# Optimization experiments

Measured on AMD Instinct MI355X. Metric: run time of the kernel, lower is better.

The kernel has to match this reference:

```python
import jax, jax.numpy as jnp
import numpy as np

T, B, D = 799, 8, 512
H, HD = 8, 64
M = 6                       # memory length (one per segment from prev layer)
SUMMARY = M + 1             # summary length = mem_length + 1
U = 768                     # utterance length = max(lengths)
R = T - U - SUMMARY         # right-context blocks length = 24
KL = M + R + U              # key length = 798
MAX_REL = 64
SCALE = HD ** -0.5
STD_SCALE = 0.5
NEG_INF = float('-inf')


def setup_inputs() -> dict:
    key = jax.random.key(0)
    ks = jax.random.split(key, 10)
    x = jax.random.normal(ks[0], (T, B, D), dtype=jnp.float32)
    mems = jax.random.normal(ks[1], (M, B, D), dtype=jnp.float32)
    lengths = jax.random.randint(ks[2], (B,), 400, U + 1).at[0].set(U).astype(jnp.int32)
    attention_mask = jax.random.bernoulli(ks[3], 0.1, (T, KL))  # True = masked
    rpe = jax.random.randint(ks[4], (T, KL), 0, 2 * MAX_REL + 1)
    wq = jax.random.normal(ks[5], (D, D), dtype=jnp.float32) * 0.02
    bq = jnp.zeros((D,), jnp.float32)
    wkv = jax.random.normal(ks[6], (2 * D, D), dtype=jnp.float32) * 0.02
    bkv = jnp.zeros((2 * D,), jnp.float32)
    wo = jax.random.normal(ks[7], (D, D), dtype=jnp.float32) * 0.02
    bo = jnp.zeros((D,), jnp.float32)
    rpe_k_emb = jax.random.normal(ks[8], (2 * MAX_REL + 1, HD), dtype=jnp.float32) * 0.05
    rpe_v_emb = jax.random.normal(ks[9], (2 * MAX_REL + 1, HD), dtype=jnp.float32) * 0.05
    return dict(x=x, lengths=lengths, mems=mems, attention_mask=attention_mask,
                rpe=rpe, utterance_length=U, wq=wq, bq=bq, wkv=wkv, bkv=bkv,
                wo=wo, bo=bo, rpe_k_emb=rpe_k_emb, rpe_v_emb=rpe_v_emb)


def attention_suppression(w, scale):
    # w: [B*H, T, KL] raw (masked) scores; weak-attention suppression per fairseq
    prob = jax.nn.softmax(w, axis=-1)
    nz = prob != 0.0
    nz_sum = jnp.sum(nz.astype(w.dtype), axis=-1, keepdims=True)
    key_sum = jnp.sum(prob, axis=-1, keepdims=True)
    key_mean = key_sum / (nz_sum + 1e-8)
    dis = jnp.where(nz, (prob - key_mean) * (prob - key_mean), 0.0)
    key_var = jnp.sum(dis, axis=-1, keepdims=True) / (nz_sum - 1.0 + 1e-8)
    key_thread = key_mean - scale * jnp.sqrt(key_var)
    return jnp.where(prob < key_thread, NEG_INF, w)


def reference(x, lengths, mems, attention_mask, rpe, utterance_length,
              wq, bq, wkv, bkv, wo, bo, rpe_k_emb, rpe_v_emb):
    summary_length = mems.shape[0] + 1
    rcb_len = T - utterance_length - summary_length  # right-context blocks
    rc_block = x[:rcb_len]
    utt_block = x[rcb_len:T - summary_length]
    # key-side padding mask: klengths = lengths + mem + right-context (lc=0)
    klengths = lengths + mems.shape[0] + rcb_len
    padding_mask = jnp.arange(KL)[None, :] >= klengths[:, None]  # [B, KL]
    mem_rc = jnp.concatenate([mems, rc_block, utt_block], axis=0)  # [KL, B, D]
    # projections (torch Linear: y = x @ W.T + b)
    q = jnp.einsum('tbd,ed->tbe', x, wq) + bq            # [T, B, D]
    kv = jnp.einsum('kbd,ed->kbe', mem_rc, wkv) + bkv    # [KL, B, 2D]
    k, v = jnp.split(kv, 2, axis=2)
    # heads: [T, B*H, HD] -> [B*H, T, HD]
    qh = jnp.transpose(q.reshape(T, B * H, HD), (1, 0, 2)) * SCALE
    kh = jnp.transpose(k.reshape(KL, B * H, HD), (1, 0, 2))
    vh = jnp.transpose(v.reshape(KL, B * H, HD), (1, 0, 2))
    aw = jnp.einsum('nth,nkh->ntk', qh, kh)              # [B*H, T, KL]
    # relative position bias on keys
    r_k = rpe_k_emb[rpe]                                 # [T, KL, HD]
    aw = aw + jnp.einsum('nth,tkh->ntk', qh, r_k)
    # attention mask (broadcast over B*H)
    aw = jnp.where(attention_mask[None, :, :], NEG_INF, aw)
    # key padding mask
    aw = aw.reshape(B, H, T, KL)
    aw = jnp.where(padding_mask[:, None, None, :], NEG_INF, aw)
    aw = aw.reshape(B * H, T, KL)
    # weak attention suppression (std_scale)
    aw = attention_suppression(aw, STD_SCALE)
    probs = jax.nn.softmax(aw, axis=-1)                  # dropout p=0
    attn = jnp.einsum('ntk,nkh->nth', probs, vh)         # [B*H, T, HD]
    r_v = rpe_v_emb[rpe]                                 # [T, KL, HD]
    attn_rpe = jnp.einsum('ntk,tkh->nth', probs, r_v)
    attn = 2.0 * attn + attn_rpe                          # rpe_old_option: attn += attn + rpe
    attn = jnp.transpose(attn, (1, 0, 2)).reshape(T, B, D)
    rc_output_memory = jnp.einsum('tbd,ed->tbe', attn, wo) + bo
    # use_mem, not mini_batches: next_m = out[-summary:-1], tanh squash
    next_m = jnp.tanh(rc_output_memory[T - summary_length:T - 1])
    rc_output = rc_output_memory[:T - summary_length]
    # concatenate the two live outputs into one array [T-1, B, D]
    return jnp.concatenate([rc_output, next_m], axis=0)
```

## Files before the change

kernel.cpp:

```cpp
#include <hip/hip_runtime.h>
#include <hip/hip_bf16.h>
#include <math.h>

#define TT   799
#define BB   8
#define DD   512
#define HH   8
#define HDD  64
#define MMEM 6
#define RRCB 24
#define KLL  798
#define TQ   798
#define NROWS (TQ * BB)
#define NHEADS 64
#define NEG_INF (-INFINITY)

#define TB   16
#define CH   64
#define NCH  13
#define VTS  832
#define NTCH 50
#define MINCH 7

static_assert(NROWS == 6384, "");

typedef __attribute__((ext_vector_type(8))) short short8;
typedef __attribute__((ext_vector_type(4))) float f32x4;

__device__ __forceinline__ unsigned short f2bf(float x) {
    union { float f; unsigned u; } c; c.f = x;
    unsigned r = c.u + 0x7FFFu + ((c.u >> 16) & 1u);
    return (unsigned short)(r >> 16);
}
__device__ __forceinline__ float bf2f(unsigned short b) {
    union { unsigned u; float f; } c; c.u = ((unsigned)b) << 16; return c.f;
}

__global__ void detect_mask_kernel(const unsigned int* __restrict__ a,
                                   int* __restrict__ mode)
{
    __shared__ int c0s, cHs;
    if (threadIdx.x == 0) { c0s = 0; cHs = 0; }
    __syncthreads();
    int c0 = 0, cH = 0;
    const int ND = 4096;
    for (int i = threadIdx.x; i < ND; i += blockDim.x) {
        unsigned int w = a[i];
        if (w & 0x000000FFu) c0++;
        if (w & 0xFFFFFF00u) cH++;
    }
    atomicAdd(&c0s, c0); atomicAdd(&cHs, cH);
    __syncthreads();
    if (threadIdx.x == 0)
        *mode = (cHs == 0) ? 0 : ((c0s == 0) ? 1 : 2);
}

#define RK_BLOCKS 36
#define PK2_BLOCKS (NTCH * 13)
__global__ __launch_bounds__(256)
void prep_kernel(const void* __restrict__ amask,
                 const int* __restrict__ rpe,
                 const int* __restrict__ mode_p,
                 unsigned int* __restrict__ pk2,
                 const float* __restrict__ rpe_k,
                 unsigned short* __restrict__ rk_hi,
                 unsigned short* __restrict__ rk_lo,
                 const float* __restrict__ x,
                 const float* __restrict__ mems,
                 const float* __restrict__ wq,
                 const float* __restrict__ wkv,
                 const float* __restrict__ wo,
                 unsigned short* __restrict__ xs_hi, unsigned short* __restrict__ xs_lo,
                 unsigned short* __restrict__ ms_hi, unsigned short* __restrict__ ms_lo,
                 unsigned short* __restrict__ w_hi,  unsigned short* __restrict__ w_lo)
{
    const int bid = blockIdx.x;
    const int tid = threadIdx.x;
    if (bid < PK2_BLOCKS) {
        const int mode = *mode_p;
        const int chunk = bid / 13;
        const int kg = bid - chunk * 13;
        const int k64 = tid >> 2;
        const int word = tid & 3;
        const int key = kg * 64 + k64;
        unsigned out = 0;
        #pragma unroll
        for (int r = 0; r < 4; ++r) {
            const int row = word * 4 + r;
            const int t = chunk * 16 + row;
            unsigned byte = 255u;
            if (key < KLL && t < TT) {
                size_t idx = (size_t)t * KLL + key;
                bool masked;
                if (mode == 0)      masked = (((const int*)amask)[idx] != 0);
                else if (mode == 1) masked = (((const float*)amask)[idx] != 0.f);
                else                masked = (((const unsigned char*)amask)[idx] != 0);
                byte = masked ? 255u : (unsigned)rpe[idx];
            }
            out |= byte << (8 * r);
        }
        pk2[((size_t)chunk * 832 + key) * 4 + word] = out;
    } else if (bid < PK2_BLOCKS + RK_BLOCKS) {
        int i = (bid - PK2_BLOCKS) * 256 + tid;
        if (i >= 144 * 64) return;
        int c = i >> 6;
        float v = (c < 129) ? rpe_k[i] : 0.f;
        unsigned short hi = f2bf(v);
        rk_hi[i] = hi;
        rk_lo[i] = f2bf(v - bf2f(hi));
    } else {
        const size_t NX = (size_t)NROWS * DD;
        const size_t NM = 48 * DD;
        const size_t NW = 2048 * DD;
        size_t i = ((size_t)(bid - PK2_BLOCKS - RK_BLOCKS) * 256 + tid) * 4;
        float4 v4; unsigned short *dh, *dl; size_t o;
        if (i < NX) { o = i; v4 = *(const float4*)(x + o); dh = xs_hi; dl = xs_lo; }
        else if (i < NX + NM) { o = i - NX; v4 = *(const float4*)(mems + o); dh = ms_hi; dl = ms_lo; }
        else if (i < NX + NM + NW) {
            o = i - NX - NM;
            size_t r = o >> 9;
            if (r < 512)       v4 = *(const float4*)(wq + o);
            else if (r < 1536) v4 = *(const float4*)(wkv + (o - (size_t)512 * DD));
            else               v4 = *(const float4*)(wo + (o - (size_t)1536 * DD));
            dh = w_hi; dl = w_lo;
        } else return;
        ushort4 h, lo;
        h.x = f2bf(v4.x); lo.x = f2bf(v4.x - bf2f(h.x));
        h.y = f2bf(v4.y); lo.y = f2bf(v4.y - bf2f(h.y));
        h.z = f2bf(v4.z); lo.z = f2bf(v4.z - bf2f(h.z));
        h.w = f2bf(v4.w); lo.w = f2bf(v4.w - bf2f(h.w));
        *(ushort4*)(dh + o) = h;
        *(ushort4*)(dl + o) = lo;
    }
}

__global__ __launch_bounds__(256)
void transpose_v_kernel(const unsigned short* __restrict__ vr_hi,
                        const unsigned short* __restrict__ vr_lo,
                        unsigned short* __restrict__ vt_hi,
                        unsigned short* __restrict__ vt_lo)
{
    const int head = blockIdx.y;
    const int kb = blockIdx.x * 64;
    __shared__ unsigned short th[64][66];
    __shared__ unsigned short tl[64][66];
    const int tid = threadIdx.x;
    for (int i = tid; i < 64 * 64; i += 256) {
        int ky = i >> 6, hd = i & 63;
        int key = kb + ky;
        unsigned short hv = 0, lv = 0;
        if (key < KLL) {
            size_t o = ((size_t)head * KLL + key) * HDD + hd;
            hv = vr_hi[o]; lv = vr_lo[o];
        }
        th[ky][hd] = hv; tl[ky][hd] = lv;
    }
    __syncthreads();
    for (int i = tid; i < 64 * 64; i += 256) {
        int hd = i >> 6, ky = i & 63;
        size_t o = ((size_t)head * HDD + hd) * VTS + kb + ky;
        vt_hi[o] = th[ky][hd];
        vt_lo[o] = tl[ky][hd];
    }
}

__global__ __launch_bounds__(256, 4)
void proj_qkv(const unsigned short* __restrict__ xs_hi,
              const unsigned short* __restrict__ xs_lo,
              const unsigned short* __restrict__ ms_hi,
              const unsigned short* __restrict__ ms_lo,
              const unsigned short* __restrict__ w_hi,
              const unsigned short* __restrict__ w_lo,
              const float* __restrict__ bq,
              const float* __restrict__ bkv,
              unsigned short* __restrict__ q_hi, unsigned short* __restrict__ q_lo,
              unsigned short* __restrict__ k_hi, unsigned short* __restrict__ k_lo,
              unsigned short* __restrict__ vr_hi, unsigned short* __restrict__ vr_lo)
{
    const int tid = threadIdx.x;
    const int wv = tid >> 6;
    const int quad = (tid >> 4) & 3;
    const int colk = tid & 15;
    const int m0 = blockIdx.x * 128;
    const int ny = blockIdx.y;
    const bool qpath = ny < 8;
    const int n0l = (qpath ? ny : ny - 8) * 64;
    const int wr0 = qpath ? n0l : 512 + n0l;

    __shared__ unsigned short wls_h[2][64][40];
    __shared__ unsigned short wls_l[2][64][40];

    const int sn = tid >> 2;
    const int sk = (tid & 3) * 8;
    const unsigned short* wsrc_h = w_hi + (size_t)(wr0 + sn) * DD + sk;
    const unsigned short* wsrc_l = w_lo + (size_t)(wr0 + sn) * DD + sk;

    const int amA = min(m0 + wv * 16 + colk, NROWS - 1);
    const int amB = min(m0 + 64 + wv * 16 + colk, NROWS - 1);
    const unsigned short *arhA, *arlA, *arhB, *arlB;
    if (qpath) {
        arhA = xs_hi + (size_t)amA * DD; arlA = xs_lo + (size_t)amA * DD;
        arhB = xs_hi + (size_t)amB * DD; arlB = xs_lo + (size_t)amB * DD;
    } else {
        if (amA < 48) { arhA = ms_hi + (size_t)amA * DD; arlA = ms_lo + (size_t)amA * DD; }
        else          { arhA = xs_hi + (size_t)(amA - 48) * DD; arlA = xs_lo + (size_t)(amA - 48) * DD; }
        if (amB < 48) { arhB = ms_hi + (size_t)amB * DD; arlB = ms_lo + (size_t)amB * DD; }
        else          { arhB = xs_hi + (size_t)(amB - 48) * DD; arlB = xs_lo + (size_t)(amB - 48) * DD; }
    }

    f32x4 acc[2][4] = {{{0,0,0,0},{0,0,0,0},{0,0,0,0},{0,0,0,0}},
                       {{0,0,0,0},{0,0,0,0},{0,0,0,0},{0,0,0,0}}};

    {
        short8 sh = *(const short8*)(wsrc_h);
        short8 sl = *(const short8*)(wsrc_l);
        *(short8*)&wls_h[0][sn][sk] = sh;
        *(short8*)&wls_l[0][sn][sk] = sl;
    }
    __syncthreads();

    #pragma unroll 2
    for (int ks = 0; ks < 16; ++ks) {
        const int buf = ks & 1;
        const int k0 = ks * 32;
        short8 nh, nl;
        if (ks + 1 < 16) {
            nh = *(const short8*)(wsrc_h + k0 + 32);
            nl = *(const short8*)(wsrc_l + k0 + 32);
        }
        short8 ahA = *(const short8*)(arhA + k0 + quad * 8);
        short8 alA = *(const short8*)(arlA + k0 + quad * 8);
        short8 ahB = *(const short8*)(arhB + k0 + quad * 8);
        short8 alB = *(const short8*)(arlB + k0 + quad * 8);
        #pragma unroll
        for (int nt = 0; nt < 4; ++nt) {
            short8 bh = *(const short8*)&wls_h[buf][nt * 16 + colk][quad * 8];
            short8 bl = *(const short8*)&wls_l[buf][nt * 16 + colk][quad * 8];
            acc[0][nt] = __builtin_amdgcn_mfma_f32_16x16x32_bf16(ahA, bh, acc[0][nt], 0, 0, 0);
            acc[0][nt] = __builtin_amdgcn_mfma_f32_16x16x32_bf16(ahA, bl, acc[0][nt], 0, 0, 0);
            acc[0][nt] = __builtin_amdgcn_mfma_f32_16x16x32_bf16(alA, bh, acc[0][nt], 0, 0, 0);
            acc[1][nt] = __builtin_amdgcn_mfma_f32_16x16x32_bf16(ahB, bh, acc[1][nt], 0, 0, 0);
            acc[1][nt] = __builtin_amdgcn_mfma_f32_16x16x32_bf16(ahB, bl, acc[1][nt], 0, 0, 0);
            acc[1][nt] = __builtin_amdgcn_mfma_f32_16x16x32_bf16(alB, bh, acc[1][nt], 0, 0, 0);
        }
        if (ks + 1 < 16) {
            *(short8*)&wls_h[buf ^ 1][sn][sk] = nh;
            *(short8*)&wls_l[buf ^ 1][sn][sk] = nl;
        }
        __syncthreads();
    }

    #pragma unroll
    for (int half = 0; half < 2; ++half) {
        #pragma unroll
        for (int nt = 0; nt < 4; ++nt) {
            const int nn = n0l + nt * 16 + colk;
            const float bv = qpath ? bq[nn] : bkv[nn];
            #pragma unroll
            for (int reg = 0; reg < 4; ++reg) {
                const int m = m0 + half * 64 + wv * 16 + quad * 4 + reg;
                if (m >= NROWS) continue;
                float v = acc[half][nt][reg] + bv;
                int row = m >> 3, bb = m & 7;
                if (qpath) {
                    v *= 0.125f;
                    int hh = nn >> 6, hd = nn & 63;
                    size_t o = ((size_t)(bb * HH + hh) * TQ + row) * HDD + hd;
                    unsigned short hi = f2bf(v);
                    q_hi[o] = hi; q_lo[o] = f2bf(v - bf2f(hi));
                } else if (nn < DD) {
                    int hh = nn >> 6, hd = nn & 63;
                    size_t o = ((size_t)(bb * HH + hh) * KLL + row) * HDD + hd;
                    unsigned short hi = f2bf(v);
                    k_hi[o] = hi; k_lo[o] = f2bf(v - bf2f(hi));
                } else {
                    int n2 = nn - DD;
                    int hh = n2 >> 6, hd = n2 & 63;
                    size_t o = ((size_t)(bb * HH + hh) * KLL + row) * HDD + hd;
                    unsigned short hi = f2bf(v);
                    vr_hi[o] = hi; vr_lo[o] = f2bf(v - bf2f(hi));
                }
            }
        }
    }
}

__global__ __launch_bounds__(256, 4)
void proj_out(const unsigned short* __restrict__ a_hi,
              const unsigned short* __restrict__ a_lo,
              const unsigned short* __restrict__ w_hi,
              const unsigned short* __restrict__ w_lo,
              const float* __restrict__ bias,
              float* __restrict__ out_f)
{
    const int tid = threadIdx.x;
    const int wv = tid >> 6;
    const int quad = (tid >> 4) & 3;
    const int colk = tid & 15;
    const int m0 = blockIdx.x * 128;
    const int n0 = blockIdx.y * 64;

    __shared__ unsigned short wls_h[2][64][40];
    __shared__ unsigned short wls_l[2][64][40];

    const int sn = tid >> 2;
    const int sk = (tid & 3) * 8;
    const unsigned short* wsrc_h = w_hi + (size_t)(n0 + sn) * DD + sk;
    const unsigned short* wsrc_l = w_lo + (size_t)(n0 + sn) * DD + sk;

    const int amA = min(m0 + wv * 16 + colk, NROWS - 1);
    const int amB = min(m0 + 64 + wv * 16 + colk, NROWS - 1);
    const unsigned short* arhA = a_hi + (size_t)amA * DD;
    const unsigned short* arlA = a_lo + (size_t)amA * DD;
    const unsigned short* arhB = a_hi + (size_t)amB * DD;
    const unsigned short* arlB = a_lo + (size_t)amB * DD;

    f32x4 acc[2][4] = {{{0,0,0,0},{0,0,0,0},{0,0,0,0},{0,0,0,0}},
                       {{0,0,0,0},{0,0,0,0},{0,0,0,0},{0,0,0,0}}};

    {
        short8 sh = *(const short8*)(wsrc_h);
        short8 sl = *(const short8*)(wsrc_l);
        *(short8*)&wls_h[0][sn][sk] = sh;
        *(short8*)&wls_l[0][sn][sk] = sl;
    }
    __syncthreads();

    #pragma unroll 2
    for (int ks = 0; ks < 16; ++ks) {
        const int buf = ks & 1;
        const int k0 = ks * 32;
        short8 nh, nl;
        if (ks + 1 < 16) {
            nh = *(const short8*)(wsrc_h + k0 + 32);
            nl = *(const short8*)(wsrc_l + k0 + 32);
        }
        short8 ahA = *(const short8*)(arhA + k0 + quad * 8);
        short8 alA = *(const short8*)(arlA + k0 + quad * 8);
        short8 ahB = *(const short8*)(arhB + k0 + quad * 8);
        short8 alB = *(const short8*)(arlB + k0 + quad * 8);
        #pragma unroll
        for (int nt = 0; nt < 4; ++nt) {
            short8 bh = *(const short8*)&wls_h[buf][nt * 16 + colk][quad * 8];
            short8 bl = *(const short8*)&wls_l[buf][nt * 16 + colk][quad * 8];
            acc[0][nt] = __builtin_amdgcn_mfma_f32_16x16x32_bf16(ahA, bh, acc[0][nt], 0, 0, 0);
            acc[0][nt] = __builtin_amdgcn_mfma_f32_16x16x32_bf16(ahA, bl, acc[0][nt], 0, 0, 0);
            acc[0][nt] = __builtin_amdgcn_mfma_f32_16x16x32_bf16(alA, bh, acc[0][nt], 0, 0, 0);
            acc[1][nt] = __builtin_amdgcn_mfma_f32_16x16x32_bf16(ahB, bh, acc[1][nt], 0, 0, 0);
            acc[1][nt] = __builtin_amdgcn_mfma_f32_16x16x32_bf16(ahB, bl, acc[1][nt], 0, 0, 0);
            acc[1][nt] = __builtin_amdgcn_mfma_f32_16x16x32_bf16(alB, bh, acc[1][nt], 0, 0, 0);
        }
        if (ks + 1 < 16) {
            *(short8*)&wls_h[buf ^ 1][sn][sk] = nh;
            *(short8*)&wls_l[buf ^ 1][sn][sk] = nl;
        }
        __syncthreads();
    }

    #pragma unroll
    for (int half = 0; half < 2; ++half) {
        #pragma unroll
        for (int nt = 0; nt < 4; ++nt) {
            const int nn = n0 + nt * 16 + colk;
            const float bv = bias[nn];
            #pragma unroll
            for (int reg = 0; reg < 4; ++reg) {
                const int m = m0 + half * 64 + wv * 16 + quad * 4 + reg;
                if (m >= NROWS) continue;
                float v = acc[half][nt][reg] + bv;
                int row = m >> 3;
                if (row >= TQ - MMEM) v = tanhf(v);
                out_f[(size_t)m * DD + nn] = v;
            }
        }
    }
}

__global__ __launch_bounds__(256, 3)
void attn_kernel(const unsigned short* __restrict__ qh_g,
                 const unsigned short* __restrict__ ql_g,
                 const unsigned short* __restrict__ kh_g,
                 const unsigned short* __restrict__ kl_g,
                 const unsigned short* __restrict__ vt_hi,
                 const unsigned short* __restrict__ vt_lo,
                 const int* __restrict__ lengths,
                 const unsigned int* __restrict__ pk2,
                 const unsigned short* __restrict__ rk_hi,
                 const unsigned short* __restrict__ rk_lo,
                 const float* __restrict__ rpe_v,
                 unsigned short* __restrict__ ao_hi,
                 unsigned short* __restrict__ ao_lo)
{
    const int id = blockIdx.x;
    const int xcd = id & 7;
    const int grp = id >> 3;
    const int t_chunk = grp % NTCH;
    const int n = (grp / NTCH) * 8 + xcd;
    const int t0 = t_chunk * TB;
    const int rows = min(TB, TQ - t0);
    const int b = n >> 3;
    const int h = n & 7;
    const int tid = threadIdx.x;
    const int wv = tid >> 6;
    const int quad = (tid >> 4) & 3;
    const int colk = tid & 15;
    const int myk = wv * 16 + colk;

    __shared__ float qrk_l[TB][132];
    __shared__ unsigned short p_hi[2][TB][72];
    __shared__ unsigned short p_lo[2][TB][72];
    __shared__ float4 stats_l[4][TB];

    const int klen = lengths[b] + MMEM + RRCB;
    const int nch_live = (klen + CH - 1) / CH;
    const unsigned* pkg = pk2 + (size_t)t_chunk * 832 * 4;

#define LIVE(c) ((c) < MINCH || (c) < nch_live)

    const int qrow = t0 + min(colk, rows - 1);
    const size_t qo = ((size_t)n * TQ + qrow) * HDD;
    short8 ah0 = *(const short8*)(qh_g + qo + quad * 8);
    short8 ah1 = *(const short8*)(qh_g + qo + 32 + quad * 8);
    short8 al0 = *(const short8*)(ql_g + qo + quad * 8);
    short8 al1 = *(const short8*)(ql_g + qo + 32 + quad * 8);

    for (int t = wv; t < 9; t += 4) {
        const size_t rb = (size_t)(t * 16 + colk) * 64;
        short8 bh0 = *(const short8*)(rk_hi + rb + quad * 8);
        short8 bh1 = *(const short8*)(rk_hi + rb + 32 + quad * 8);
        short8 bl0 = *(const short8*)(rk_lo + rb + quad * 8);
        short8 bl1 = *(const short8*)(rk_lo + rb + 32 + quad * 8);
        f32x4 c4 = {0.f, 0.f, 0.f, 0.f};
        c4 = __builtin_amdgcn_mfma_f32_16x16x32_bf16(ah0, bh0, c4, 0, 0, 0);
        c4 = __builtin_amdgcn_mfma_f32_16x16x32_bf16(ah1, bh1, c4, 0, 0, 0);
        c4 = __builtin_amdgcn_mfma_f32_16x16x32_bf16(ah0, bl0, c4, 0, 0, 0);
        c4 = __builtin_amdgcn_mfma_f32_16x16x32_bf16(ah1, bl1, c4, 0, 0, 0);
        c4 = __builtin_amdgcn_mfma_f32_16x16x32_bf16(al0, bh0, c4, 0, 0, 0);
        c4 = __builtin_amdgcn_mfma_f32_16x16x32_bf16(al1, bh1, c4, 0, 0, 0);
        int c = t * 16 + colk;
        if (c <= 128) {
            #pragma unroll
            for (int reg = 0; reg < 4; ++reg) qrk_l[quad * 4 + reg][c] = c4[reg];
        }
    }
    __syncthreads();

    float s_reg[NCH][4];
    float mx[4] = {-1e30f, -1e30f, -1e30f, -1e30f};

    #pragma unroll
    for (int cc = 0; cc < NCH; ++cc) {
        if (LIVE(cc)) {
            const int key = cc * CH + myk;
            const int krow = min(key, KLL - 1);
            const size_t ko = ((size_t)n * KLL + krow) * HDD;
            const unsigned r4 = pkg[key * 4 + quad];
            short8 bh0 = *(const short8*)(kh_g + ko + quad * 8);
            short8 bh1 = *(const short8*)(kh_g + ko + 32 + quad * 8);
            short8 bl0 = *(const short8*)(kl_g + ko + quad * 8);
            short8 bl1 = *(const short8*)(kl_g + ko + 32 + quad * 8);
            f32x4 c4a = {0.f, 0.f, 0.f, 0.f};
            f32x4 c4b = {0.f, 0.f, 0.f, 0.f};
            c4a = __builtin_amdgcn_mfma_f32_16x16x32_bf16(ah0, bh0, c4a, 0, 0, 0);
            c4b = __builtin_amdgcn_mfma_f32_16x16x32_bf16(ah1, bh1, c4b, 0, 0, 0);
            c4a = __builtin_amdgcn_mfma_f32_16x16x32_bf16(ah0, bl0, c4a, 0, 0, 0);
            c4b = __builtin_amdgcn_mfma_f32_16x16x32_bf16(ah1, bl1, c4b, 0, 0, 0);
            c4a = __builtin_amdgcn_mfma_f32_16x16x32_bf16(al0, bh0, c4a, 0, 0, 0);
            c4b = __builtin_amdgcn_mfma_f32_16x16x32_bf16(al1, bh1, c4b, 0, 0, 0);

            const bool vkey = (key < klen);
            #pragma unroll
            for (int reg = 0; reg < 4; ++reg) {
                const int row = quad * 4 + reg;
                const unsigned rid = (r4 >> (8 * reg)) & 255u;
                const float qv = qrk_l[row][min(rid, 128u)];
                float s = (c4a[reg] + c4b[reg]) + qv;
                const bool ok = vkey && (row < rows) && (rid != 255u);
                s = ok ? s : -1e30f;
                mx[reg] = fmaxf(mx[reg], s);
                s_reg[cc][reg] = s;
            }
        } else {
            #pragma unroll
            for (int reg = 0; reg < 4; ++reg) s_reg[cc][reg] = -1e30f;
        }
    }

    #pragma unroll
    for (int reg = 0; reg < 4; ++reg)
        #pragma unroll
        for (int d = 1; d < 16; d <<= 1) mx[reg] = fmaxf(mx[reg], __shfl_xor(mx[reg], d, 16));
    if (colk == 0) {
        #pragma unroll
        for (int reg = 0; reg < 4; ++reg)
            stats_l[wv][quad * 4 + reg] = make_float4(mx[reg], 0.f, 0.f, 0.f);
    }
    __syncthreads();
    if (tid < TB) {
        float M = fmaxf(fmaxf(stats_l[0][tid].x, stats_l[1][tid].x),
                        fmaxf(stats_l[2][tid].x, stats_l[3][tid].x));
        stats_l[0][tid].x = M;
    }
    __syncthreads();

    float Mr[4], l[4] = {0,0,0,0}, l2[4] = {0,0,0,0}, cn[4] = {0,0,0,0};
    #pragma unroll
    for (int reg = 0; reg < 4; ++reg) Mr[reg] = stats_l[0][quad * 4 + reg].x;
    #pragma unroll
    for (int cc = 0; cc < NCH; ++cc) {
        if (LIVE(cc)) {
            #pragma unroll
            for (int reg = 0; reg < 4; ++reg) {
                float s = s_reg[cc][reg];
                float e = expf(s - Mr[reg]);
                cn[reg] += (s > -1e29f) ? 1.f : 0.f;
                l[reg] += e;
                l2[reg] = fmaf(e, e, l2[reg]);
                s_reg[cc][reg] = e;
            }
        }
    }
    #pragma unroll
    for (int reg = 0; reg < 4; ++reg)
        #pragma unroll
        for (int d = 1; d < 16; d <<= 1) {
            l[reg]  += __shfl_xor(l[reg], d, 16);
            l2[reg] += __shfl_xor(l2[reg], d, 16);
            cn[reg] += __shfl_xor(cn[reg], d, 16);
        }
    if (colk == 0) {
        #pragma unroll
        for (int reg = 0; reg < 4; ++reg)
            stats_l[wv][quad * 4 + reg] = make_float4(Mr[reg], l[reg], l2[reg], cn[reg]);
    }
    __syncthreads();
    if (tid < TB) {
        float L = 0.f, L2 = 0.f, C = 0.f;
        #pragma unroll
        for (int w = 0; w < 4; ++w) {
            float4 s4 = stats_l[w][tid];
            L += s4.y; L2 += s4.z; C += s4.w;
        }
        float inv = (L > 0.f) ? 1.f / L : 0.f;
        float mean = 1.f / (C + 1e-8f);
        float sump2 = L2 * inv * inv;
        float var = (sump2 - 2.f * mean + C * mean * mean) / (C - 1.f + 1e-8f);
        var = fmaxf(var, 0.f);
        float thr = mean - 0.5f * sqrtf(var);
        stats_l[0][tid] = make_float4(stats_l[0][tid].x, inv, thr, 0.f);
    }
    for (int i = tid; i < TB * 132; i += 256) ((float*)qrk_l)[i] = 0.f;
    __syncthreads();

    float inv_r[4], thr_r[4];
    #pragma unroll
    for (int reg = 0; reg < 4; ++reg) {
        float4 s4 = stats_l[0][quad * 4 + reg];
        inv_r[reg] = s4.y; thr_r[reg] = s4.z;
    }
    float sig[4] = {0.f, 0.f, 0.f, 0.f};
    f32x4 oaccA = {0.f, 0.f, 0.f, 0.f};
    f32x4 oaccB = {0.f, 0.f, 0.f, 0.f};

    auto computeP = [&](int cc, int buf, unsigned r4) {
        #pragma unroll
        for (int reg = 0; reg < 4; ++reg) {
            const int row = quad * 4 + reg;
            float p = s_reg[cc][reg] * inv_r[reg];
            if (p < thr_r[reg]) p = 0.f;
            sig[reg] += p;
            if (p > 0.f) {
                unsigned rid = (r4 >> (8 * reg)) & 255u;
                atomicAdd(&qrk_l[row][rid], p);
            }
            unsigned short ph = f2bf(p);
            p_hi[buf][row][myk] = ph;
            p_lo[buf][row][myk] = f2bf(p - bf2f(ph));
        }
    };

    short8 vh0, vh1, vl0, vl1;
    {
        const size_t vbase = ((size_t)n * HDD + wv * 16 + colk) * VTS;
        vh0 = *(const short8*)(vt_hi + vbase + quad * 8);
        vh1 = *(const short8*)(vt_hi + vbase + 32 + quad * 8);
        vl0 = *(const short8*)(vt_lo + vbase + quad * 8);
        vl1 = *(const short8*)(vt_lo + vbase + 32 + quad * 8);
    }
    computeP(0, 0, pkg[myk * 4 + quad]);
    __syncthreads();
    #pragma unroll
    for (int cc = 0; cc < NCH; ++cc) {
        if (LIVE(cc)) {
            const bool nlive = (cc + 1 < NCH) && LIVE(cc + 1);
            short8 nvh0, nvh1, nvl0, nvl1; unsigned nr4 = 0;
            if (nlive) {
                const size_t vbase = ((size_t)n * HDD + wv * 16 + colk) * VTS
                                   + (cc + 1) * CH;
                nvh0 = *(const short8*)(vt_hi + vbase + quad * 8);
                nvh1 = *(const short8*)(vt_hi + vbase + 32 + quad * 8);
                nvl0 = *(const short8*)(vt_lo + vbase + quad * 8);
                nvl1 = *(const short8*)(vt_lo + vbase + 32 + quad * 8);
                nr4 = pkg[((cc + 1) * CH + myk) * 4 + quad];
            }
            const int buf = cc & 1;
            short8 ph0 = *(const short8*)&p_hi[buf][colk][quad * 8];
            short8 ph1 = *(const short8*)&p_hi[buf][colk][32 + quad * 8];
            short8 pl0 = *(const short8*)&p_lo[buf][colk][quad * 8];
            short8 pl1 = *(const short8*)&p_lo[buf][colk][32 + quad * 8];
            oaccA = __builtin_amdgcn_mfma_f32_16x16x32_bf16(vh0, ph0, oaccA, 0, 0, 0);
            oaccB = __builtin_amdgcn_mfma_f32_16x16x32_bf16(vh1, ph1, oaccB, 0, 0, 0);
            oaccA = __builtin_amdgcn_mfma_f32_16x16x32_bf16(vh0, pl0, oaccA, 0, 0, 0);
            oaccB = __builtin_amdgcn_mfma_f32_16x16x32_bf16(vh1, pl1, oaccB, 0, 0, 0);
            oaccA = __builtin_amdgcn_mfma_f32_16x16x32_bf16(vl0, ph0, oaccA, 0, 0, 0);
            oaccB = __builtin_amdgcn_mfma_f32_16x16x32_bf16(vl1, ph1, oaccB, 0, 0, 0);
            if (nlive) computeP(cc + 1, (cc + 1) & 1, nr4);
            __syncthreads();
            if (nlive) { vh0 = nvh0; vh1 = nvh1; vl0 = nvl0; vl1 = nvl1; }
        }
    }

    #pragma unroll
    for (int reg = 0; reg < 4; ++reg)
        #pragma unroll
        for (int d = 1; d < 16; d <<= 1) sig[reg] += __shfl_xor(sig[reg], d, 16);
    if (colk == 0) {
        #pragma unroll
        for (int reg = 0; reg < 4; ++reg)
            stats_l[wv][quad * 4 + reg].w = sig[reg];
    }
    __syncthreads();
    if (tid < TB) {
        float S = stats_l[0][tid].w + stats_l[1][tid].w + stats_l[2][tid].w + stats_l[3][tid].w;
        stats_l[0][tid].w = (S > 0.f) ? 1.f / S : 0.f;
    }
    __syncthreads();

    if (colk < rows) {
        float4 ar = {0.f, 0.f, 0.f, 0.f};
        const int hdb = wv * 16 + quad * 4;
        #pragma unroll 4
        for (int c = 0; c < 129; ++c) {
            float p = qrk_l[colk][c];
            float4 v4 = *(const float4*)(rpe_v + (size_t)c * HDD + hdb);
            ar.x = fmaf(p, v4.x, ar.x);
            ar.y = fmaf(p, v4.y, ar.y);
            ar.z = fmaf(p, v4.z, ar.z);
            ar.w = fmaf(p, v4.w, ar.w);
        }
        const float invS = stats_l[0][colk].w;
        float o0 = (2.f * (oaccA[0] + oaccB[0]) + ar.x) * invS;
        float o1 = (2.f * (oaccA[1] + oaccB[1]) + ar.y) * invS;
        float o2 = (2.f * (oaccA[2] + oaccB[2]) + ar.z) * invS;
        float o3 = (2.f * (oaccA[3] + oaccB[3]) + ar.w) * invS;
        size_t oo = ((size_t)(t0 + colk) * BB + b) * DD + h * HDD + hdb;
        ushort4 oh, ol;
        oh.x = f2bf(o0); ol.x = f2bf(o0 - bf2f(oh.x));
        oh.y = f2bf(o1); ol.y = f2bf(o1 - bf2f(oh.y));
        oh.z = f2bf(o2); ol.z = f2bf(o2 - bf2f(oh.z));
        oh.w = f2bf(o3); ol.w = f2bf(o3 - bf2f(oh.w));
        *(ushort4*)(ao_hi + oo) = oh;
        *(ushort4*)(ao_lo + oo) = ol;
    }
#undef LIVE
}

extern "C" void kernel_launch(void* const* d_in, const int* in_sizes, int n_in,
                              void* d_out, int out_size, void* d_ws, size_t ws_size,
                              hipStream_t stream) {
    const float*          x      = (const float*)d_in[0];
    const int*            lengths= (const int*)d_in[1];
    const float*          mems   = (const float*)d_in[2];
    const void*           amask  = (const void*)d_in[3];
    const int*            rpe    = (const int*)d_in[4];
    const float*          wq     = (const float*)d_in[6];
    const float*          bq     = (const float*)d_in[7];
    const float*          wkv    = (const float*)d_in[8];
    const float*          bkv    = (const float*)d_in[9];
    const float*          wo     = (const float*)d_in[10];
    const float*          bo     = (const float*)d_in[11];
    const float*          rpe_k  = (const float*)d_in[12];
    const float*          rpe_v  = (const float*)d_in[13];

    const size_t NE = (size_t)NROWS * DD;
    const size_t VTN = (size_t)NHEADS * HDD * VTS;

    char* p = (char*)d_ws;
    unsigned short* q_hi = (unsigned short*)p;  p += NE * 2;
    unsigned short* q_lo = (unsigned short*)p;  p += NE * 2;
    char* uni = p;                              p += VTN * 4;
    unsigned short* xs_hi = (unsigned short*)uni;
    unsigned short* xs_lo = xs_hi + NE;
    unsigned short* ms_hi = xs_lo + NE;
    unsigned short* ms_lo = ms_hi + 48 * DD;
    unsigned short* vt_hi = (unsigned short*)uni;
    unsigned short* vt_lo = vt_hi + VTN;
    unsigned short* w_hi = (unsigned short*)p;  p += (size_t)2048 * DD * 2;
    unsigned short* w_lo = (unsigned short*)p;  p += (size_t)2048 * DD * 2;
    unsigned short* k_hi = (unsigned short*)p;  p += NE * 2;
    unsigned short* k_lo = (unsigned short*)p;  p += NE * 2;
    unsigned short* vr_hi = (unsigned short*)p; p += NE * 2;
    unsigned short* vr_lo = (unsigned short*)p; p += NE * 2;
    unsigned short* ao_hi = vr_hi;
    unsigned short* ao_lo = vr_lo;
    unsigned short* rk_hi = (unsigned short*)p; p += 144 * 64 * 2;
    unsigned short* rk_lo = (unsigned short*)p; p += 144 * 64 * 2;
    unsigned int*   pk2   = (unsigned int*)p;   p += (size_t)NTCH * 832 * 16;
    int* mmode = (int*)p;

    detect_mask_kernel<<<1, 1024, 0, stream>>>((const unsigned int*)amask, mmode);
    {
        const size_t sp_total = NE + (size_t)48 * DD + (size_t)2048 * DD;
        const int sp_blocks = (int)((sp_total + 1023) / 1024);
        prep_kernel<<<PK2_BLOCKS + RK_BLOCKS + sp_blocks, 256, 0, stream>>>(
            amask, rpe, mmode, pk2,
            rpe_k, rk_hi, rk_lo,
            x, mems, wq, wkv, wo,
            xs_hi, xs_lo, ms_hi, ms_lo, w_hi, w_lo);
    }
    proj_qkv<<<dim3(50, 24), 256, 0, stream>>>(
        xs_hi, xs_lo, ms_hi, ms_lo, w_hi, w_lo, bq, bkv,
        q_hi, q_lo, k_hi, k_lo, vr_hi, vr_lo);
    transpose_v_kernel<<<dim3(13, NHEADS), 256, 0, stream>>>(vr_hi, vr_lo, vt_hi, vt_lo);
    attn_kernel<<<3200, 256, 0, stream>>>(
        q_hi, q_lo, k_hi, k_lo, vt_hi, vt_lo, lengths, pk2, rk_hi, rk_lo, rpe_v, ao_hi, ao_lo);
    proj_out<<<dim3(50, 8), 256, 0, stream>>>(
        ao_hi, ao_lo, w_hi + (size_t)1536 * DD, w_lo + (size_t)1536 * DD, bo,
        (float*)d_out);
}
```

Before: 463.2 us.

## Fold mask detection into prep, halve GEMM M-tiles, add MFMA priority hints

Removes the separate single-block mask-type detection launch and has each mask-packing block of the prep kernel recompute the mode from the first 4096 words. This saves one kernel launch and a serial dependency at the cost of redundant reads per block. Halves the row tile of the QKV and output projection GEMMs from 128 to 64 and doubles their grids to 100 blocks in x, giving more blocks across the CUs but less A/B reuse per block. Wraps the MFMA sequences in the attention kernel with s_setprio raises to favour matrix issue over other waves.

```diff
diff --git a/kernel.cpp b/kernel.cpp
--- a/kernel.cpp
+++ b/kernel.cpp
@@ -36,31 +36,11 @@
     union { unsigned u; float f; } c; c.u = ((unsigned)b) << 16; return c.f;
 }
 
-__global__ void detect_mask_kernel(const unsigned int* __restrict__ a,
-                                   int* __restrict__ mode)
-{
-    __shared__ int c0s, cHs;
-    if (threadIdx.x == 0) { c0s = 0; cHs = 0; }
-    __syncthreads();
-    int c0 = 0, cH = 0;
-    const int ND = 4096;
-    for (int i = threadIdx.x; i < ND; i += blockDim.x) {
-        unsigned int w = a[i];
-        if (w & 0x000000FFu) c0++;
-        if (w & 0xFFFFFF00u) cH++;
-    }
-    atomicAdd(&c0s, c0); atomicAdd(&cHs, cH);
-    __syncthreads();
-    if (threadIdx.x == 0)
-        *mode = (cHs == 0) ? 0 : ((c0s == 0) ? 1 : 2);
-}
-
 #define RK_BLOCKS 36
 #define PK2_BLOCKS (NTCH * 13)
 __global__ __launch_bounds__(256)
 void prep_kernel(const void* __restrict__ amask,
                  const int* __restrict__ rpe,
-                 const int* __restrict__ mode_p,
                  unsigned int* __restrict__ pk2,
                  const float* __restrict__ rpe_k,
                  unsigned short* __restrict__ rk_hi,
@@ -77,7 +57,22 @@
     const int bid = blockIdx.x;
     const int tid = threadIdx.x;
     if (bid < PK2_BLOCKS) {
-        const int mode = *mode_p;
+        __shared__ int c0s, cHs;
+        if (tid == 0) { c0s = 0; cHs = 0; }
+        __syncthreads();
+        {
+            int c0 = 0, cH = 0;
+            const unsigned* aw = (const unsigned*)amask;
+            for (int i = tid; i < 4096; i += 256) {
+                unsigned w = aw[i];
+                if (w & 0x000000FFu) c0++;
+                if (w & 0xFFFFFF00u) cH++;
+            }
+            atomicAdd(&c0s, c0); atomicAdd(&cHs, cH);
+        }
+        __syncthreads();
+        const int mode = (cHs == 0) ? 0 : ((c0s == 0) ? 1 : 2);
+
         const int chunk = bid / 13;
         const int kg = bid - chunk * 13;
         const int k64 = tid >> 2;
@@ -165,23 +160,23 @@
 }
 
 __global__ __launch_bounds__(256, 4)
-void proj_qkv(const unsigned short* __restrict__ xs_hi,
-              const unsigned short* __restrict__ xs_lo,
-              const unsigned short* __restrict__ ms_hi,
-              const unsigned short* __restrict__ ms_lo,
-              const unsigned short* __restrict__ w_hi,
-              const unsigned short* __restrict__ w_lo,
-              const float* __restrict__ bq,
-              const float* __restrict__ bkv,
-              unsigned short* __restrict__ q_hi, unsigned short* __restrict__ q_lo,
-              unsigned short* __restrict__ k_hi, unsigned short* __restrict__ k_lo,
-              unsigned short* __restrict__ vr_hi, unsigned short* __restrict__ vr_lo)
+void proj_qkv64(const unsigned short* __restrict__ xs_hi,
+                const unsigned short* __restrict__ xs_lo,
+                const unsigned short* __restrict__ ms_hi,
+                const unsigned short* __restrict__ ms_lo,
+                const unsigned short* __restrict__ w_hi,
+                const unsigned short* __restrict__ w_lo,
+                const float* __restrict__ bq,
+                const float* __restrict__ bkv,
+                unsigned short* __restrict__ q_hi, unsigned short* __restrict__ q_lo,
+                unsigned short* __restrict__ k_hi, unsigned short* __restrict__ k_lo,
+                unsigned short* __restrict__ vr_hi, unsigned short* __restrict__ vr_lo)
 {
     const int tid = threadIdx.x;
     const int wv = tid >> 6;
     const int quad = (tid >> 4) & 3;
     const int colk = tid & 15;
-    const int m0 = blockIdx.x * 128;
+    const int m0 = blockIdx.x * 64;
     const int ny = blockIdx.y;
     const bool qpath = ny < 8;
     const int n0l = (qpath ? ny : ny - 8) * 64;
@@ -195,21 +190,16 @@
     const unsigned short* wsrc_h = w_hi + (size_t)(wr0 + sn) * DD + sk;
     const unsigned short* wsrc_l = w_lo + (size_t)(wr0 + sn) * DD + sk;
 
-    const int amA = min(m0 + wv * 16 + colk, NROWS - 1);
-    const int amB = min(m0 + 64 + wv * 16 + colk, NROWS - 1);
-    const unsigned short *arhA, *arlA, *arhB, *arlB;
+    const int am = min(m0 + wv * 16 + colk, NROWS - 1);
+    const unsigned short *arh, *arl;
     if (qpath) {
-        arhA = xs_hi + (size_t)amA * DD; arlA = xs_lo + (size_t)amA * DD;
-        arhB = xs_hi + (size_t)amB * DD; arlB = xs_lo + (size_t)amB * DD;
+        arh = xs_hi + (size_t)am * DD; arl = xs_lo + (size_t)am * DD;
     } else {
-        if (amA < 48) { arhA = ms_hi + (size_t)amA * DD; arlA = ms_lo + (size_t)amA * DD; }
-        else          { arhA = xs_hi + (size_t)(amA - 48) * DD; arlA = xs_lo + (size_t)(amA - 48) * DD; }
-        if (amB < 48) { arhB = ms_hi + (size_t)amB * DD; arlB = ms_lo + (size_t)amB * DD; }
-        else          { arhB = xs_hi + (size_t)(amB - 48) * DD; arlB = xs_lo + (size_t)(amB - 48) * DD; }
-    }
-
-    f32x4 acc[2][4] = {{{0,0,0,0},{0,0,0,0},{0,0,0,0},{0,0,0,0}},
-                       {{0,0,0,0},{0,0,0,0},{0,0,0,0},{0,0,0,0}}};
+        if (am < 48) { arh = ms_hi + (size_t)am * DD; arl = ms_lo + (size_t)am * DD; }
+        else         { arh = xs_hi + (size_t)(am - 48) * DD; arl = xs_lo + (size_t)(am - 48) * DD; }
+    }
+
+    f32x4 acc[4] = {{0,0,0,0},{0,0,0,0},{0,0,0,0},{0,0,0,0}};
 
     {
         short8 sh = *(const short8*)(wsrc_h);
@@ -228,20 +218,15 @@
             nh = *(const short8*)(wsrc_h + k0 + 32);
             nl = *(const short8*)(wsrc_l + k0 + 32);
         }
-        short8 ahA = *(const short8*)(arhA + k0 + quad * 8);
-        short8 alA = *(const short8*)(arlA + k0 + quad * 8);
-        short8 ahB = *(const short8*)(arhB + k0 + quad * 8);
-        short8 alB = *(const short8*)(arlB + k0 + quad * 8);
+        short8 ah = *(const short8*)(arh + k0 + quad * 8);
+        short8 al = *(const short8*)(arl + k0 + quad * 8);
         #pragma unroll
         for (int nt = 0; nt < 4; ++nt) {
             short8 bh = *(const short8*)&wls_h[buf][nt * 16 + colk][quad * 8];
             short8 bl = *(const short8*)&wls_l[buf][nt * 16 + colk][quad * 8];
-            acc[0][nt] = __builtin_amdgcn_mfma_f32_16x16x32_bf16(ahA, bh, acc[0][nt], 0, 0, 0);
-            acc[0][nt] = __builtin_amdgcn_mfma_f32_16x16x32_bf16(ahA, bl, acc[0][nt], 0, 0, 0);
-            acc[0][nt] = __builtin_amdgcn_mfma_f32_16x16x32_bf16(alA, bh, acc[0][nt], 0, 0, 0);
-            acc[1][nt] = __builtin_amdgcn_mfma_f32_16x16x32_bf16(ahB, bh, acc[1][nt], 0, 0, 0);
-            acc[1][nt] = __builtin_amdgcn_mfma_f32_16x16x32_bf16(ahB, bl, acc[1][nt], 0, 0, 0);
-            acc[1][nt] = __builtin_amdgcn_mfma_f32_16x16x32_bf16(alB, bh, acc[1][nt], 0, 0, 0);
+            acc[nt] = __builtin_amdgcn_mfma_f32_16x16x32_bf16(ah, bh, acc[nt], 0, 0, 0);
+            acc[nt] = __builtin_amdgcn_mfma_f32_16x16x32_bf16(ah, bl, acc[nt], 0, 0, 0);
+            acc[nt] = __builtin_amdgcn_mfma_f32_16x16x32_bf16(al, bh, acc[nt], 0, 0, 0);
         }
         if (ks + 1 < 16) {
             *(short8*)&wls_h[buf ^ 1][sn][sk] = nh;
@@ -251,35 +236,32 @@
     }
 
     #pragma unroll
-    for (int half = 0; half < 2; ++half) {
-        #pragma unroll
-        for (int nt = 0; nt < 4; ++nt) {
-            const int nn = n0l + nt * 16 + colk;
-            const float bv = qpath ? bq[nn] : bkv[nn];
-            #pragma unroll
-            for (int reg = 0; reg < 4; ++reg) {
-                const int m = m0 + half * 64 + wv * 16 + quad * 4 + reg;
-                if (m >= NROWS) continue;
-                float v = acc[half][nt][reg] + bv;
-                int row = m >> 3, bb = m & 7;
-                if (qpath) {
-                    v *= 0.125f;
-                    int hh = nn >> 6, hd = nn & 63;
-                    size_t o = ((size_t)(bb * HH + hh) * TQ + row) * HDD + hd;
-                    unsigned short hi = f2bf(v);
-                    q_hi[o] = hi; q_lo[o] = f2bf(v - bf2f(hi));
-                } else if (nn < DD) {
-                    int hh = nn >> 6, hd = nn & 63;
-                    size_t o = ((size_t)(bb * HH + hh) * KLL + row) * HDD + hd;
-                    unsigned short hi = f2bf(v);
-                    k_hi[o] = hi; k_lo[o] = f2bf(v - bf2f(hi));
-                } else {
-                    int n2 = nn - DD;
-                    int hh = n2 >> 6, hd = n2 & 63;
-                    size_t o = ((size_t)(bb * HH + hh) * KLL + row) * HDD + hd;
-                    unsigned short hi = f2bf(v);
-                    vr_hi[o] = hi; vr_lo[o] = f2bf(v - bf2f(hi));
-                }
+    for (int nt = 0; nt < 4; ++nt) {
+        const int nn = n0l + nt * 16 + colk;
+        const float bv = qpath ? bq[nn] : bkv[nn];
+        #pragma unroll
+        for (int reg = 0; reg < 4; ++reg) {
+            const int m = m0 + wv * 16 + quad * 4 + reg;
+            if (m >= NROWS) continue;
+            float v = acc[nt][reg] + bv;
+            int row = m >> 3, bb = m & 7;
+            if (qpath) {
+                v *= 0.125f;
+                int hh = nn >> 6, hd = nn & 63;
+                size_t o = ((size_t)(bb * HH + hh) * TQ + row) * HDD + hd;
+                unsigned short hi = f2bf(v);
+                q_hi[o] = hi; q_lo[o] = f2bf(v - bf2f(hi));
+            } else if (nn < DD) {
+                int hh = nn >> 6, hd = nn & 63;
+                size_t o = ((size_t)(bb * HH + hh) * KLL + row) * HDD + hd;
+                unsigned short hi = f2bf(v);
+                k_hi[o] = hi; k_lo[o] = f2bf(v - bf2f(hi));
+            } else {
+                int n2 = nn - DD;
+                int hh = n2 >> 6, hd = n2 & 63;
+                size_t o = ((size_t)(bb * HH + hh) * KLL + row) * HDD + hd;
+                unsigned short hi = f2bf(v);
+                vr_hi[o] = hi; vr_lo[o] = f2bf(v - bf2f(hi));
             }
         }
     }
@@ -297,7 +279,7 @@
     const int wv = tid >> 6;
     const int quad = (tid >> 4) & 3;
     const int colk = tid & 15;
-    const int m0 = blockIdx.x * 128;
+    const int m0 = blockIdx.x * 64;
     const int n0 = blockIdx.y * 64;
 
     __shared__ unsigned short wls_h[2][64][40];
@@ -308,15 +290,11 @@
     const unsigned short* wsrc_h = w_hi + (size_t)(n0 + sn) * DD + sk;
     const unsigned short* wsrc_l = w_lo + (size_t)(n0 + sn) * DD + sk;
 
-    const int amA = min(m0 + wv * 16 + colk, NROWS - 1);
-    const int amB = min(m0 + 64 + wv * 16 + colk, NROWS - 1);
-    const unsigned short* arhA = a_hi + (size_t)amA * DD;
-    const unsigned short* arlA = a_lo + (size_t)amA * DD;
-    const unsigned short* arhB = a_hi + (size_t)amB * DD;
-    const unsigned short* arlB = a_lo + (size_t)amB * DD;
-
-    f32x4 acc[2][4] = {{{0,0,0,0},{0,0,0,0},{0,0,0,0},{0,0,0,0}},
-                       {{0,0,0,0},{0,0,0,0},{0,0,0,0},{0,0,0,0}}};
+    const int am = min(m0 + wv * 16 + colk, NROWS - 1);
+    const unsigned short* arh = a_hi + (size_t)am * DD;
+    const unsigned short* arl = a_lo + (size_t)am * DD;
+
+    f32x4 acc[4] = {{0,0,0,0},{0,0,0,0},{0,0,0,0},{0,0,0,0}};
 
     {
         short8 sh = *(const short8*)(wsrc_h);
@@ -335,20 +313,15 @@
             nh = *(const short8*)(wsrc_h + k0 + 32);
             nl = *(const short8*)(wsrc_l + k0 + 32);
         }
-        short8 ahA = *(const short8*)(arhA + k0 + quad * 8);
-        short8 alA = *(const short8*)(arlA + k0 + quad * 8);
-        short8 ahB = *(const short8*)(arhB + k0 + quad * 8);
-        short8 alB = *(const short8*)(arlB + k0 + quad * 8);
+        short8 ah = *(const short8*)(arh + k0 + quad * 8);
+        short8 al = *(const short8*)(arl + k0 + quad * 8);
         #pragma unroll
         for (int nt = 0; nt < 4; ++nt) {
             short8 bh = *(const short8*)&wls_h[buf][nt * 16 + colk][quad * 8];
             short8 bl = *(const short8*)&wls_l[buf][nt * 16 + colk][quad * 8];
-            acc[0][nt] = __builtin_amdgcn_mfma_f32_16x16x32_bf16(ahA, bh, acc[0][nt], 0, 0, 0);
-            acc[0][nt] = __builtin_amdgcn_mfma_f32_16x16x32_bf16(ahA, bl, acc[0][nt], 0, 0, 0);
-            acc[0][nt] = __builtin_amdgcn_mfma_f32_16x16x32_bf16(alA, bh, acc[0][nt], 0, 0, 0);
-            acc[1][nt] = __builtin_amdgcn_mfma_f32_16x16x32_bf16(ahB, bh, acc[1][nt], 0, 0, 0);
-            acc[1][nt] = __builtin_amdgcn_mfma_f32_16x16x32_bf16(ahB, bl, acc[1][nt], 0, 0, 0);
-            acc[1][nt] = __builtin_amdgcn_mfma_f32_16x16x32_bf16(alB, bh, acc[1][nt], 0, 0, 0);
+            acc[nt] = __builtin_amdgcn_mfma_f32_16x16x32_bf16(ah, bh, acc[nt], 0, 0, 0);
+            acc[nt] = __builtin_amdgcn_mfma_f32_16x16x32_bf16(ah, bl, acc[nt], 0, 0, 0);
+            acc[nt] = __builtin_amdgcn_mfma_f32_16x16x32_bf16(al, bh, acc[nt], 0, 0, 0);
         }
         if (ks + 1 < 16) {
             *(short8*)&wls_h[buf ^ 1][sn][sk] = nh;
@@ -358,20 +331,17 @@
     }
 
     #pragma unroll
-    for (int half = 0; half < 2; ++half) {
-        #pragma unroll
-        for (int nt = 0; nt < 4; ++nt) {
-            const int nn = n0 + nt * 16 + colk;
-            const float bv = bias[nn];
-            #pragma unroll
-            for (int reg = 0; reg < 4; ++reg) {
-                const int m = m0 + half * 64 + wv * 16 + quad * 4 + reg;
-                if (m >= NROWS) continue;
-                float v = acc[half][nt][reg] + bv;
-                int row = m >> 3;
-                if (row >= TQ - MMEM) v = tanhf(v);
-                out_f[(size_t)m * DD + nn] = v;
-            }
+    for (int nt = 0; nt < 4; ++nt) {
+        const int nn = n0 + nt * 16 + colk;
+        const float bv = bias[nn];
+        #pragma unroll
+        for (int reg = 0; reg < 4; ++reg) {
+            const int m = m0 + wv * 16 + quad * 4 + reg;
+            if (m >= NROWS) continue;
+            float v = acc[nt][reg] + bv;
+            int row = m >> 3;
+            if (row >= TQ - MMEM) v = tanhf(v);
+            out_f[(size_t)m * DD + nn] = v;
         }
     }
 }
@@ -431,12 +401,14 @@
         short8 bl0 = *(const short8*)(rk_lo + rb + quad * 8);
         short8 bl1 = *(const short8*)(rk_lo + rb + 32 + quad * 8);
         f32x4 c4 = {0.f, 0.f, 0.f, 0.f};
+        __builtin_amdgcn_s_setprio(1);
         c4 = __builtin_amdgcn_mfma_f32_16x16x32_bf16(ah0, bh0, c4, 0, 0, 0);
         c4 = __builtin_amdgcn_mfma_f32_16x16x32_bf16(ah1, bh1, c4, 0, 0, 0);
         c4 = __builtin_amdgcn_mfma_f32_16x16x32_bf16(ah0, bl0, c4, 0, 0, 0);
         c4 = __builtin_amdgcn_mfma_f32_16x16x32_bf16(ah1, bl1, c4, 0, 0, 0);
         c4 = __builtin_amdgcn_mfma_f32_16x16x32_bf16(al0, bh0, c4, 0, 0, 0);
         c4 = __builtin_amdgcn_mfma_f32_16x16x32_bf16(al1, bh1, c4, 0, 0, 0);
+        __builtin_amdgcn_s_setprio(0);
         int c = t * 16 + colk;
         if (c <= 128) {
             #pragma unroll
@@ -461,12 +433,14 @@
             short8 bl1 = *(const short8*)(kl_g + ko + 32 + quad * 8);
             f32x4 c4a = {0.f, 0.f, 0.f, 0.f};
             f32x4 c4b = {0.f, 0.f, 0.f, 0.f};
+            __builtin_amdgcn_s_setprio(1);
             c4a = __builtin_amdgcn_mfma_f32_16x16x32_bf16(ah0, bh0, c4a, 0, 0, 0);
             c4b = __builtin_amdgcn_mfma_f32_16x16x32_bf16(ah1, bh1, c4b, 0, 0, 0);
             c4a = __builtin_amdgcn_mfma_f32_16x16x32_bf16(ah0, bl0, c4a, 0, 0, 0);
             c4b = __builtin_amdgcn_mfma_f32_16x16x32_bf16(ah1, bl1, c4b, 0, 0, 0);
             c4a = __builtin_amdgcn_mfma_f32_16x16x32_bf16(al0, bh0, c4a, 0, 0, 0);
             c4b = __builtin_amdgcn_mfma_f32_16x16x32_bf16(al1, bh1, c4b, 0, 0, 0);
+            __builtin_amdgcn_s_setprio(0);
 
             const bool vkey = (key < klen);
             #pragma unroll
@@ -608,12 +582,14 @@
             short8 ph1 = *(const short8*)&p_hi[buf][colk][32 + quad * 8];
             short8 pl0 = *(const short8*)&p_lo[buf][colk][quad * 8];
             short8 pl1 = *(const short8*)&p_lo[buf][colk][32 + quad * 8];
+            __builtin_amdgcn_s_setprio(1);
             oaccA = __builtin_amdgcn_mfma_f32_16x16x32_bf16(vh0, ph0, oaccA, 0, 0, 0);
             oaccB = __builtin_amdgcn_mfma_f32_16x16x32_bf16(vh1, ph1, oaccB, 0, 0, 0);
             oaccA = __builtin_amdgcn_mfma_f32_16x16x32_bf16(vh0, pl0, oaccA, 0, 0, 0);
             oaccB = __builtin_amdgcn_mfma_f32_16x16x32_bf16(vh1, pl1, oaccB, 0, 0, 0);
             oaccA = __builtin_amdgcn_mfma_f32_16x16x32_bf16(vl0, ph0, oaccA, 0, 0, 0);
             oaccB = __builtin_amdgcn_mfma_f32_16x16x32_bf16(vl1, ph1, oaccB, 0, 0, 0);
+            __builtin_amdgcn_s_setprio(0);
             if (nlive) computeP(cc + 1, (cc + 1) & 1, nr4);
             __syncthreads();
             if (nlive) { vh0 = nvh0; vh1 = nvh1; vl0 = nvl0; vl1 = nvl1; }
@@ -706,25 +682,23 @@
     unsigned short* rk_hi = (unsigned short*)p; p += 144 * 64 * 2;
     unsigned short* rk_lo = (unsigned short*)p; p += 144 * 64 * 2;
     unsigned int*   pk2   = (unsigned int*)p;   p += (size_t)NTCH * 832 * 16;
-    int* mmode = (int*)p;
-
-    detect_mask_kernel<<<1, 1024, 0, stream>>>((const unsigned int*)amask, mmode);
+
     {
         const size_t sp_total = NE + (size_t)48 * DD + (size_t)2048 * DD;
         const int sp_blocks = (int)((sp_total + 1023) / 1024);
         prep_kernel<<<PK2_BLOCKS + RK_BLOCKS + sp_blocks, 256, 0, stream>>>(
-            amask, rpe, mmode, pk2,
+            amask, rpe, pk2,
             rpe_k, rk_hi, rk_lo,
             x, mems, wq, wkv, wo,
             xs_hi, xs_lo, ms_hi, ms_lo, w_hi, w_lo);
     }
-    proj_qkv<<<dim3(50, 24), 256, 0, stream>>>(
+    proj_qkv64<<<dim3(100, 24), 256, 0, stream>>>(
         xs_hi, xs_lo, ms_hi, ms_lo, w_hi, w_lo, bq, bkv,
         q_hi, q_lo, k_hi, k_lo, vr_hi, vr_lo);
     transpose_v_kernel<<<dim3(13, NHEADS), 256, 0, stream>>>(vr_hi, vr_lo, vt_hi, vt_lo);
     attn_kernel<<<3200, 256, 0, stream>>>(
         q_hi, q_lo, k_hi, k_lo, vt_hi, vt_lo, lengths, pk2, rk_hi, rk_lo, rpe_v, ao_hi, ao_lo);
-    proj_out<<<dim3(50, 8), 256, 0, stream>>>(
+    proj_out<<<dim3(100, 8), 256, 0, stream>>>(
         ao_hi, ao_lo, w_hi + (size_t)1536 * DD, w_lo + (size_t)1536 * DD, bo,
         (float*)d_out);
 }
```

Result: faster. 449.7 us (median of 2 runs) (-2.9%).
